# Performance work log

Measured on AMD Instinct MI355X. Metric: run time of the kernel, lower is better.

Reference implementation:

```python
import jax, jax.numpy as jnp
import numpy as np

N, H, S, D = 2, 8, 2048, 64

def setup_inputs() -> dict:
    key = jax.random.key(0)
    k1, k2, k3, k4 = jax.random.split(key, 4)
    queries = jax.random.normal(k1, (N, H, S, D), dtype=jnp.float32)
    keys = jax.random.normal(k2, (N, H, S, D), dtype=jnp.float32)
    values = jax.random.normal(k3, (N, H, S, D), dtype=jnp.float32)
    attn_mask = jax.random.randint(k4, (1, 1, S, S), 0, 2, dtype=jnp.int32)
    return {"queries": queries, "keys": keys, "values": values, "attn_mask": attn_mask}

def reference(queries, keys, values, attn_mask):
    # Faithful to the torch code: softmax over axis=2 (query/seq axis) for Q,
    # softmax over axis=1 (heads axis) for K, exactly as written.
    Q = jax.nn.softmax(queries, axis=2)
    K = jax.nn.softmax(keys, axis=1)
    attention_weights = jnp.einsum('nhqd,nhkd->nhqk', Q, K)  # [N,H,S,S]
    attention_weights = jnp.where(attn_mask == 0, -jnp.inf, attention_weights)
    attention_weights = jax.nn.softmax(attention_weights, axis=-1)
    context = jnp.einsum('nhqk,nhkd->nhqd', attention_weights, values)
    return context, attention_weights
```

## Files before the change

### kernel.cpp

```cpp
#include <hip/hip_runtime.h>

#define S 2048
#define Dh 64
#define NH 16
#define SD (S*Dh)
#define SSZ ((size_t)S*(size_t)S)

typedef __attribute__((ext_vector_type(4))) float f32x4;
typedef __attribute__((ext_vector_type(16))) float f32x16;
typedef __attribute__((ext_vector_type(8))) short s16x8;
typedef __attribute__((ext_vector_type(4))) unsigned int u32x4;

#define WSB_QSUM 0
#define WSB_RINV 4096
#define WSB_MASK 135168
#define WSB_QS   659456
#define WSB_KS   (WSB_QS + 4194304)
#define WSB_VT   (WSB_KS + 4194304)

__device__ __forceinline__ ushort f2bf(float x) {
    unsigned u = __builtin_bit_cast(unsigned, x);
    u = (u + 0x7fffu + ((u >> 16) & 1u)) >> 16;
    return (ushort)u;
}

__device__ __forceinline__ void gload_lds16(const ushort* g, ushort* l) {
    __builtin_amdgcn_global_load_lds(
        (const __attribute__((address_space(1))) unsigned int*)(const void*)g,
        (__attribute__((address_space(3))) unsigned int*)(void*)l,
        16, 0, 0);
}

__global__ void k_qsum(const float* __restrict__ q, float* __restrict__ qsum) {
    const int head  = blockIdx.x >> 5;
    const int chunk = blockIdx.x & 31;
    const int t = threadIdx.x;
    const int d = t & 63, sg = t >> 6;
    const float* qh = q + (size_t)head * SD;
    const int s0 = chunk * 64;
    float acc = 0.f;
#pragma unroll
    for (int i = 0; i < 16; ++i) {
        int s = s0 + sg + 4 * i;
        acc += __expf(qh[s * Dh + d]);
    }
    __shared__ float part[4][64];
    part[sg][d] = acc;
    __syncthreads();
    if (sg == 0)
        atomicAdd(&qsum[head * 64 + d], part[0][d] + part[1][d] + part[2][d] + part[3][d]);
}

__global__ void k_qnorm(const float* __restrict__ q, const float* __restrict__ qsum,
                        ushort* __restrict__ Qs) {
    const int gid = blockIdx.x * 256 + threadIdx.x;
    const int i0 = gid * 8;
    const int head = i0 >> 17;
    const int d0 = i0 & 63;
    const float4 a = ((const float4*)(q + i0))[0];
    const float4 b = ((const float4*)(q + i0))[1];
    const float* qs = qsum + head * 64 + d0;
    s16x8 o;
    o[0] = (short)f2bf(__expf(a.x) / qs[0]);
    o[1] = (short)f2bf(__expf(a.y) / qs[1]);
    o[2] = (short)f2bf(__expf(a.z) / qs[2]);
    o[3] = (short)f2bf(__expf(a.w) / qs[3]);
    o[4] = (short)f2bf(__expf(b.x) / qs[4]);
    o[5] = (short)f2bf(__expf(b.y) / qs[5]);
    o[6] = (short)f2bf(__expf(b.z) / qs[6]);
    o[7] = (short)f2bf(__expf(b.w) / qs[7]);
    *(s16x8*)(Qs + i0) = o;
}

__global__ void k_ksoft(const float* __restrict__ kin, ushort* __restrict__ Ks) {
    const int gid = blockIdx.x * 256 + threadIdx.x;
    const int n = gid >> 17;
    const int rem = gid & (SD - 1);
    const float* base = kin + (size_t)n * 8 * SD + rem;
    float x[8];
    float sum = 0.f;
#pragma unroll
    for (int h = 0; h < 8; ++h) { x[h] = __expf(base[(size_t)h * SD]); sum += x[h]; }
    const float inv = 1.f / sum;
    ushort* ob = Ks + (size_t)n * 8 * SD + rem;
#pragma unroll
    for (int h = 0; h < 8; ++h) ob[(size_t)h * SD] = f2bf(x[h] * inv);
}

__global__ void k_vt(const float* __restrict__ V, ushort* __restrict__ Vt) {
    const int head = blockIdx.x >> 5, kt = blockIdx.x & 31;
    const int t = threadIdx.x;
    __shared__ float sv[64 * 68];
    const float4* src = (const float4*)(V + (size_t)head * SD + (size_t)kt * 64 * 64);
#pragma unroll
    for (int i = 0; i < 4; ++i) {
        int idx = t + 256 * i;
        int row = idx >> 4, c4 = idx & 15;
        *(float4*)&sv[row * 68 + c4 * 4] = src[idx];
    }
    __syncthreads();
    const int d = t >> 2, seg = t & 3;
    s16x8 v0, v1;
#pragma unroll
    for (int j = 0; j < 8; ++j) v0[j] = (short)f2bf(sv[(seg * 16 + j) * 68 + d]);
#pragma unroll
    for (int j = 0; j < 8; ++j) v1[j] = (short)f2bf(sv[(seg * 16 + 8 + j) * 68 + d]);
    ushort* dst = Vt + (size_t)head * SD + (size_t)d * S + kt * 64 + seg * 16;
    *(s16x8*)dst = v0;
    *(s16x8*)(dst + 8) = v1;
}

__global__ void k_mask(const int* __restrict__ mask, unsigned long long* __restrict__ bmt) {
    const int t = threadIdx.x;
    const int g = blockIdx.x * 4 + (t >> 6);
    const int lane = t & 63;
#pragma unroll
    for (int it = 0; it < 16; ++it) {
        int w = g * 16 + it;
        int m = mask[(size_t)w * 64 + lane];
        unsigned long long b = __ballot(m != 0);
        if (lane == 0) bmt[(size_t)(w & 31) * S + (w >> 5)] = b;
    }
}

__global__ __launch_bounds__(256, 4) void k_ctx(
        const ushort* __restrict__ Qs, const ushort* __restrict__ Ks,
        const ushort* __restrict__ Vt, const unsigned long long* __restrict__ bmt,
        float* __restrict__ ctx, float* __restrict__ rinv) {
    const int head = blockIdx.x, qt = blockIdx.y;
    const int q0 = qt * 32;
    const int t = threadIdx.x;
    const int lane = t & 63, w = t >> 6;
    const int ql = lane & 31, hi = lane >> 5;
    const int q = q0 + ql;

    __shared__ __align__(16) char smem[37504];
    ushort* sK = (ushort*)smem;
    ushort* sV = (ushort*)(smem + 16384);
    float* redo  = (float*)smem;
    float* redrs = (float*)(smem + 36864);
    float* sInv  = (float*)(smem + 37376);

    const ushort* Qb = Qs + (size_t)head * SD;
    const ushort* Kb = Ks + (size_t)head * SD;
    const ushort* Vb = Vt + (size_t)head * SD;

    s16x8 bq[4];
#pragma unroll
    for (int s = 0; s < 4; ++s)
        bq[s] = *(const s16x8*)(Qb + (size_t)q * 64 + 16 * s + 8 * hi);

    f32x16 o0, o1;
#pragma unroll
    for (int r = 0; r < 16; ++r) { o0[r] = 0.f; o1[r] = 0.f; }
    float rs = 0.f;

    for (int mt = 0; mt < 16; ++mt) {
        const int k0 = mt * 128;
        __syncthreads();
#pragma unroll
        for (int i = 0; i < 4; ++i) {
            const int idx = t + 256 * i;
            const int row = idx >> 3, c = idx & 7;
            gload_lds16(Kb + (size_t)(k0 + row) * 64 + ((c ^ (row & 7)) * 8), &sK[idx * 8]);
        }
#pragma unroll
        for (int i = 0; i < 4; ++i) {
            const int idx = t + 256 * i;
            const int row = idx >> 4, c = idx & 15;
            gload_lds16(Vb + (size_t)row * S + k0 + ((c ^ (row & 7)) * 8), &sV[idx * 8]);
        }
        __syncthreads();

        f32x16 sc;
#pragma unroll
        for (int r = 0; r < 16; ++r) sc[r] = 0.f;
        const int arow = 32 * w + ql;
#pragma unroll
        for (int s = 0; s < 4; ++s) {
            const s16x8 ak = *(const s16x8*)&sK[arow * 64 + (((2 * s + hi) ^ (arow & 7)) * 8)];
            sc = __builtin_amdgcn_mfma_f32_32x32x16_bf16(ak, bq[s], sc, 0, 0, 0);
        }

        const unsigned long long m64 = bmt[(size_t)(2 * mt + (w >> 1)) * S + q];
        const unsigned mbits = (w & 1) ? (unsigned)(m64 >> 32) : (unsigned)m64;

        unsigned pk8[8];
        float rsum = 0.f;
#pragma unroll
        for (int g = 0; g < 8; ++g) {
            const int r0 = 2 * g;
            const int kb = (r0 & 3) + 8 * (r0 >> 2) + 4 * hi;
            const float e0 = ((mbits >> kb) & 1u) ? __expf(sc[r0]) : 0.f;
            const float e1 = ((mbits >> (kb + 1)) & 1u) ? __expf(sc[r0 + 1]) : 0.f;
            rsum += e0 + e1;
            pk8[g] = ((unsigned)f2bf(e1) << 16) | (unsigned)f2bf(e0);
        }
        rsum += __shfl_xor(rsum, 32);
        rs += rsum;

        const unsigned x1 = __shfl_xor(hi ? pk8[0] : pk8[2], 32);
        const unsigned x2 = __shfl_xor(hi ? pk8[1] : pk8[3], 32);
        const unsigned x3 = __shfl_xor(hi ? pk8[4] : pk8[6], 32);
        const unsigned x4 = __shfl_xor(hi ? pk8[5] : pk8[7], 32);
        const u32x4 w0 = hi ? (u32x4){x1, x2, pk8[2], pk8[3]}
                            : (u32x4){pk8[0], pk8[1], x1, x2};
        const u32x4 w1 = hi ? (u32x4){x3, x4, pk8[6], pk8[7]}
                            : (u32x4){pk8[4], pk8[5], x3, x4};
        const s16x8 pb0 = __builtin_bit_cast(s16x8, w0);
        const s16x8 pb1 = __builtin_bit_cast(s16x8, w1);

#pragma unroll
        for (int cs = 0; cs < 2; ++cs) {
            const s16x8 pbv = cs ? pb1 : pb0;
            {
                const int vrow = ql;
                const int ch = (4 * w + 2 * cs + hi) ^ (vrow & 7);
                const s16x8 av = *(const s16x8*)&sV[vrow * 128 + ch * 8];
                o0 = __builtin_amdgcn_mfma_f32_32x32x16_bf16(av, pbv, o0, 0, 0, 0);
            }
            {
                const int vrow = 32 + ql;
                const int ch = (4 * w + 2 * cs + hi) ^ (vrow & 7);
                const s16x8 av = *(const s16x8*)&sV[vrow * 128 + ch * 8];
                o1 = __builtin_amdgcn_mfma_f32_32x32x16_bf16(av, pbv, o1, 0, 0, 0);
            }
        }
    }

    __syncthreads();
    {
        float* dst = &redo[(w * 64 + lane) * 36];
#pragma unroll
        for (int g = 0; g < 4; ++g)
            *(f32x4*)&dst[4 * g] = (f32x4){o0[4*g], o0[4*g+1], o0[4*g+2], o0[4*g+3]};
#pragma unroll
        for (int g = 0; g < 4; ++g)
            *(f32x4*)&dst[16 + 4 * g] = (f32x4){o1[4*g], o1[4*g+1], o1[4*g+2], o1[4*g+3]};
        if (hi == 0) redrs[w * 32 + ql] = rs;
    }
    __syncthreads();
    if (t < 32) {
        const float inv = 1.f / (redrs[t] + redrs[32 + t] + redrs[64 + t] + redrs[96 + t]);
        rinv[head * S + q0 + t] = inv;
        sInv[t] = inv;
    }
    __syncthreads();
#pragma unroll
    for (int cc = 0; cc < 2; ++cc) {
        const int c = t + 256 * cc;
        const int l = c & 63, rq = c >> 6;
        f32x4 sum = *(const f32x4*)&redo[l * 36 + rq * 4];
#pragma unroll
        for (int ww = 1; ww < 4; ++ww)
            sum += *(const f32x4*)&redo[(ww * 64 + l) * 36 + rq * 4];
        const int qc = l & 31, hc = l >> 5;
        const int dtc = rq >> 2, rg = rq & 3;
        const int d0 = 32 * dtc + 4 * hc + 8 * rg;
        sum *= sInv[qc];
        *(f32x4*)(ctx + (size_t)head * SD + (size_t)(q0 + qc) * 64 + d0) = sum;
    }
}

__global__ __launch_bounds__(256, 4) void k_awrite(
        const ushort* __restrict__ Qs, const ushort* __restrict__ Ks,
        const unsigned long long* __restrict__ bmt, const float* __restrict__ rinv,
        float* __restrict__ A) {
    const int head = blockIdx.x, qt = blockIdx.y, kc = blockIdx.z;
    const int q0 = qt * 64;
    const int t = threadIdx.x;
    const int lane = t & 63, wv = t >> 6;
    const int lm = lane & 15, lg = lane >> 4;
    const int q = q0 + 16 * wv + lm;

    __shared__ __align__(16) char smem[33792];
    ushort* sK = (ushort*)smem;
    float* sP = (float*)(smem + 16384);

    const ushort* Qb = Qs + (size_t)head * SD;
    const ushort* Kb = Ks + (size_t)head * SD;
    float* Ah = A + (size_t)head * SSZ;

    auto stage = [&](int b, int k0) {
#pragma unroll
        for (int i = 0; i < 2; ++i) {
            const int idx = t + 256 * i;
            const int row = idx >> 3, seg = idx & 7;
            gload_lds16(Kb + (size_t)(k0 + row) * 64 + ((seg ^ (row & 7)) * 8),
                        &sK[b * 4096 + idx * 8]);
        }
    };

    s16x8 bq[2];
#pragma unroll
    for (int h = 0; h < 2; ++h)
        bq[h] = *(const s16x8*)(Qb + (size_t)q * 64 + 32 * h + 8 * lg);
    const float invr = rinv[head * S + q];
    float* sPw = &sP[wv * 16 * 68];

    stage(0, kc * 512);
    unsigned long long m64 = bmt[(size_t)(kc * 8) * S + q];
    __syncthreads();

    for (int kt8 = 0; kt8 < 8; ++kt8) {
        const int k0 = kc * 512 + kt8 * 64;
        const int cur = kt8 & 1;
        if (kt8 < 7) stage(cur ^ 1, k0 + 64);
        const unsigned long long m64n =
            (kt8 < 7) ? bmt[(size_t)((k0 >> 6) + 1) * S + q] : 0ULL;

        f32x4 sc[4];
#pragma unroll
        for (int j = 0; j < 4; ++j) sc[j] = (f32x4){0.f, 0.f, 0.f, 0.f};
#pragma unroll
        for (int h = 0; h < 2; ++h)
#pragma unroll
            for (int j = 0; j < 4; ++j) {
                s16x8 ak = *(const s16x8*)&sK[cur * 4096 + (16 * j + lm) * 64 +
                                              (((4 * h + lg) ^ (lm & 7)) * 8)];
                sc[j] = __builtin_amdgcn_mfma_f32_16x16x32_bf16(ak, bq[h], sc[j], 0, 0, 0);
            }

#pragma unroll
        for (int j = 0; j < 4; ++j) {
            f32x4 pv;
#pragma unroll
            for (int r = 0; r < 4; ++r) {
                const int b = 16 * j + 4 * lg + r;
                pv[r] = ((m64 >> b) & 1ULL) ? __expf(sc[j][r]) * invr : 0.f;
            }
            *(f32x4*)&sPw[lm * 68 + 16 * j + 4 * lg] = pv;
        }
#pragma unroll
        for (int pass = 0; pass < 4; ++pass) {
            const int rr = (lane >> 4) + 4 * pass;
            f32x4 pv = *(const f32x4*)&sPw[rr * 68 + (lane & 15) * 4];
            __builtin_nontemporal_store(pv,
                (f32x4*)&Ah[(size_t)(q0 + 16 * wv + rr) * S + k0 + (lane & 15) * 4]);
        }
        __syncthreads();
        m64 = m64n;
    }
}

extern "C" void kernel_launch(void* const* d_in, const int* in_sizes, int n_in,
                              void* d_out, int out_size, void* d_ws, size_t ws_size,
                              hipStream_t stream) {
    const float* q = (const float*)d_in[0];
    const float* k = (const float*)d_in[1];
    const float* v = (const float*)d_in[2];
    const int* mask = (const int*)d_in[3];
    float* out = (float*)d_out;
    char* ws = (char*)d_ws;

    float* qsum = (float*)(ws + WSB_QSUM);
    float* rinv = (float*)(ws + WSB_RINV);
    unsigned long long* bm = (unsigned long long*)(ws + WSB_MASK);
    ushort* Qs = (ushort*)(ws + WSB_QS);
    ushort* Ks = (ushort*)(ws + WSB_KS);
    ushort* Vt = (ushort*)(ws + WSB_VT);

    (void)hipMemsetAsync(d_ws, 0, 4096, stream);
    k_qsum<<<512, 256, 0, stream>>>(q, qsum);
    k_mask<<<1024, 256, 0, stream>>>(mask, bm);
    k_qnorm<<<1024, 256, 0, stream>>>(q, qsum, Qs);
    k_ksoft<<<1024, 256, 0, stream>>>(k, Ks);
    k_vt<<<512, 256, 0, stream>>>(v, Vt);
    k_ctx<<<dim3(16, 64), 256, 0, stream>>>(Qs, Ks, Vt, bm, out, rinv);
    k_awrite<<<dim3(16, 32, 4), 256, 0, stream>>>(Qs, Ks, bm, rinv, out + (size_t)NH * SD);
}
```

Before: 377.0 us.

## Store unnormalized bf16 probabilities in ctx kernel and rescale them for attention output

The ctx kernel now also writes its masked, exponentiated bf16 scores to a workspace buffer. The attention-weights kernel no longer recomputes QK^T with MFMA, the exp and the mask. It reads those packed values, multiplies them by the row inverse sum, transposes them through LDS and stores them in fp32. This trades a second pass of matrix math for an extra 128 MB of bf16 traffic (a write and a read), and it adds stores inside ctx's inner loop.

```diff
diff --git a/kernel.cpp b/kernel.cpp
--- a/kernel.cpp
+++ b/kernel.cpp
@@ -17,6 +17,7 @@
 #define WSB_QS   659456
 #define WSB_KS   (WSB_QS + 4194304)
 #define WSB_VT   (WSB_KS + 4194304)
+#define WSB_PR   13242368
 
 __device__ __forceinline__ ushort f2bf(float x) {
     unsigned u = __builtin_bit_cast(unsigned, x);
@@ -126,7 +127,7 @@
 __global__ __launch_bounds__(256, 4) void k_ctx(
         const ushort* __restrict__ Qs, const ushort* __restrict__ Ks,
         const ushort* __restrict__ Vt, const unsigned long long* __restrict__ bmt,
-        float* __restrict__ ctx, float* __restrict__ rinv) {
+        unsigned* __restrict__ Pr, float* __restrict__ ctx, float* __restrict__ rinv) {
     const int head = blockIdx.x, qt = blockIdx.y;
     const int q0 = qt * 32;
     const int t = threadIdx.x;
@@ -195,6 +196,12 @@
             const float e1 = ((mbits >> (kb + 1)) & 1u) ? __expf(sc[r0 + 1]) : 0.f;
             rsum += e0 + e1;
             pk8[g] = ((unsigned)f2bf(e1) << 16) | (unsigned)f2bf(e0);
+        }
+        {
+            unsigned* dst = Pr + ((size_t)head << 21) + ((size_t)qt << 15)
+                               + (mt << 11) + (w << 9) + lane * 4;
+            *(u32x4*)dst = (u32x4){pk8[0], pk8[1], pk8[2], pk8[3]};
+            *(u32x4*)(dst + 256) = (u32x4){pk8[4], pk8[5], pk8[6], pk8[7]};
         }
         rsum += __shfl_xor(rsum, 32);
         rs += rsum;
@@ -262,84 +269,46 @@
     }
 }
 
-__global__ __launch_bounds__(256, 4) void k_awrite(
-        const ushort* __restrict__ Qs, const ushort* __restrict__ Ks,
-        const unsigned long long* __restrict__ bmt, const float* __restrict__ rinv,
+__global__ __launch_bounds__(256, 8) void k_ascale(
+        const unsigned* __restrict__ Pr, const float* __restrict__ rinv,
         float* __restrict__ A) {
-    const int head = blockIdx.x, qt = blockIdx.y, kc = blockIdx.z;
-    const int q0 = qt * 64;
+    const int head = blockIdx.x, qg = blockIdx.y, kc = blockIdx.z;
+    const int q0 = qg * 32;
     const int t = threadIdx.x;
     const int lane = t & 63, wv = t >> 6;
-    const int lm = lane & 15, lg = lane >> 4;
-    const int q = q0 + 16 * wv + lm;
-
-    __shared__ __align__(16) char smem[33792];
-    ushort* sK = (ushort*)smem;
-    float* sP = (float*)(smem + 16384);
-
-    const ushort* Qb = Qs + (size_t)head * SD;
-    const ushort* Kb = Ks + (size_t)head * SD;
+    const int ql = lane & 31, lh = lane >> 5;
+
+    __shared__ __align__(16) float sPf[32][132];
+
+    const float invr = rinv[head * S + q0 + ql];
     float* Ah = A + (size_t)head * SSZ;
-
-    auto stage = [&](int b, int k0) {
-#pragma unroll
-        for (int i = 0; i < 2; ++i) {
-            const int idx = t + 256 * i;
-            const int row = idx >> 3, seg = idx & 7;
-            gload_lds16(Kb + (size_t)(k0 + row) * 64 + ((seg ^ (row & 7)) * 8),
-                        &sK[b * 4096 + idx * 8]);
-        }
-    };
-
-    s16x8 bq[2];
-#pragma unroll
-    for (int h = 0; h < 2; ++h)
-        bq[h] = *(const s16x8*)(Qb + (size_t)q * 64 + 32 * h + 8 * lg);
-    const float invr = rinv[head * S + q];
-    float* sPw = &sP[wv * 16 * 68];
-
-    stage(0, kc * 512);
-    unsigned long long m64 = bmt[(size_t)(kc * 8) * S + q];
-    __syncthreads();
-
-    for (int kt8 = 0; kt8 < 8; ++kt8) {
-        const int k0 = kc * 512 + kt8 * 64;
-        const int cur = kt8 & 1;
-        if (kt8 < 7) stage(cur ^ 1, k0 + 64);
-        const unsigned long long m64n =
-            (kt8 < 7) ? bmt[(size_t)((k0 >> 6) + 1) * S + q] : 0ULL;
-
-        f32x4 sc[4];
-#pragma unroll
-        for (int j = 0; j < 4; ++j) sc[j] = (f32x4){0.f, 0.f, 0.f, 0.f};
-#pragma unroll
-        for (int h = 0; h < 2; ++h)
-#pragma unroll
-            for (int j = 0; j < 4; ++j) {
-                s16x8 ak = *(const s16x8*)&sK[cur * 4096 + (16 * j + lm) * 64 +
-                                              (((4 * h + lg) ^ (lm & 7)) * 8)];
-                sc[j] = __builtin_amdgcn_mfma_f32_16x16x32_bf16(ak, bq[h], sc[j], 0, 0, 0);
-            }
-
+    const unsigned* baseh = Pr + ((size_t)head << 21) + ((size_t)qg << 15);
+
+    for (int m = 0; m < 8; ++m) {
+        const int mt = kc * 8 + m;
+        const unsigned* bb = baseh + (mt << 11) + (wv << 9);
+        const u32x4 a = *(const u32x4*)(bb + (32 * lh + ql) * 4);
+        const u32x4 b = *(const u32x4*)(bb + 256 + (32 * lh + ql) * 4);
 #pragma unroll
         for (int j = 0; j < 4; ++j) {
-            f32x4 pv;
-#pragma unroll
-            for (int r = 0; r < 4; ++r) {
-                const int b = 16 * j + 4 * lg + r;
-                pv[r] = ((m64 >> b) & 1ULL) ? __expf(sc[j][r]) * invr : 0.f;
-            }
-            *(f32x4*)&sPw[lm * 68 + 16 * j + 4 * lg] = pv;
-        }
-#pragma unroll
-        for (int pass = 0; pass < 4; ++pass) {
-            const int rr = (lane >> 4) + 4 * pass;
-            f32x4 pv = *(const f32x4*)&sPw[rr * 68 + (lane & 15) * 4];
-            __builtin_nontemporal_store(pv,
-                (f32x4*)&Ah[(size_t)(q0 + 16 * wv + rr) * S + k0 + (lane & 15) * 4]);
+            const unsigned ga = (j == 0) ? a[0] : (j == 1) ? a[2] : (j == 2) ? b[0] : b[2];
+            const unsigned gb = (j == 0) ? a[1] : (j == 1) ? a[3] : (j == 2) ? b[1] : b[3];
+            f32x4 v;
+            v[0] = __builtin_bit_cast(float, ga << 16) * invr;
+            v[1] = __builtin_bit_cast(float, ga & 0xFFFF0000u) * invr;
+            v[2] = __builtin_bit_cast(float, gb << 16) * invr;
+            v[3] = __builtin_bit_cast(float, gb & 0xFFFF0000u) * invr;
+            *(f32x4*)&sPf[ql][wv * 32 + 8 * j + 4 * lh] = v;
         }
         __syncthreads();
-        m64 = m64n;
+#pragma unroll
+        for (int rr = 0; rr < 4; ++rr) {
+            const int row = rr * 8 + (t >> 5);
+            const f32x4 vv = *(const f32x4*)&sPf[row][(t & 31) * 4];
+            __builtin_nontemporal_store(vv,
+                (f32x4*)&Ah[(size_t)(q0 + row) * S + mt * 128 + (t & 31) * 4]);
+        }
+        __syncthreads();
     }
 }
 
@@ -359,6 +328,7 @@
     ushort* Qs = (ushort*)(ws + WSB_QS);
     ushort* Ks = (ushort*)(ws + WSB_KS);
     ushort* Vt = (ushort*)(ws + WSB_VT);
+    unsigned* Pr = (unsigned*)(ws + WSB_PR);
 
     (void)hipMemsetAsync(d_ws, 0, 4096, stream);
     k_qsum<<<512, 256, 0, stream>>>(q, qsum);
@@ -366,6 +336,6 @@
     k_qnorm<<<1024, 256, 0, stream>>>(q, qsum, Qs);
     k_ksoft<<<1024, 256, 0, stream>>>(k, Ks);
     k_vt<<<512, 256, 0, stream>>>(v, Vt);
-    k_ctx<<<dim3(16, 64), 256, 0, stream>>>(Qs, Ks, Vt, bm, out, rinv);
-    k_awrite<<<dim3(16, 32, 4), 256, 0, stream>>>(Qs, Ks, bm, rinv, out + (size_t)NH * SD);
-}
+    k_ctx<<<dim3(16, 64), 256, 0, stream>>>(Qs, Ks, Vt, bm, Pr, out, rinv);
+    k_ascale<<<dim3(16, 64, 2), 256, 0, stream>>>(Pr, rinv, out + (size_t)NH * SD);
+}
```

Result: slower. 387.4 us (+2.8%).

## Single-buffer K tile and stage probabilities as bf16 to raise awrite occupancy

Applied to the files above, without the earlier changes.

The attention-weight write kernel drops K double buffering and stores the probability tile in shared memory as packed bf16 instead of fp32. This shrinks LDS per block from about 33KB to 17KB, and launch bounds are raised from 4 to 6 blocks per CU. Each thread now writes 64 contiguous bytes per row when it expands the bf16 values back to fp32 for the nontemporal stores. In exchange, K loads for the next tile are no longer overlapped with compute, and the written attention weights are rounded to bf16 precision, which may exceed tolerance.

```diff
diff --git a/kernel.cpp b/kernel.cpp
--- a/kernel.cpp
+++ b/kernel.cpp
@@ -262,7 +262,7 @@
     }
 }
 
-__global__ __launch_bounds__(256, 4) void k_awrite(
+__global__ __launch_bounds__(256, 6) void k_awrite(
         const ushort* __restrict__ Qs, const ushort* __restrict__ Ks,
         const unsigned long long* __restrict__ bmt, const float* __restrict__ rinv,
         float* __restrict__ A) {
@@ -273,21 +273,21 @@
     const int lm = lane & 15, lg = lane >> 4;
     const int q = q0 + 16 * wv + lm;
 
-    __shared__ __align__(16) char smem[33792];
+    __shared__ __align__(16) char smem[17408];
     ushort* sK = (ushort*)smem;
-    float* sP = (float*)(smem + 16384);
+    unsigned* sP = (unsigned*)(smem + 8192);
 
     const ushort* Qb = Qs + (size_t)head * SD;
     const ushort* Kb = Ks + (size_t)head * SD;
     float* Ah = A + (size_t)head * SSZ;
 
-    auto stage = [&](int b, int k0) {
+    auto stage = [&](int k0) {
 #pragma unroll
         for (int i = 0; i < 2; ++i) {
             const int idx = t + 256 * i;
             const int row = idx >> 3, seg = idx & 7;
             gload_lds16(Kb + (size_t)(k0 + row) * 64 + ((seg ^ (row & 7)) * 8),
-                        &sK[b * 4096 + idx * 8]);
+                        &sK[idx * 8]);
         }
     };
 
@@ -296,18 +296,13 @@
     for (int h = 0; h < 2; ++h)
         bq[h] = *(const s16x8*)(Qb + (size_t)q * 64 + 32 * h + 8 * lg);
     const float invr = rinv[head * S + q];
-    float* sPw = &sP[wv * 16 * 68];
-
-    stage(0, kc * 512);
+
+    stage(kc * 512);
     unsigned long long m64 = bmt[(size_t)(kc * 8) * S + q];
-    __syncthreads();
 
     for (int kt8 = 0; kt8 < 8; ++kt8) {
         const int k0 = kc * 512 + kt8 * 64;
-        const int cur = kt8 & 1;
-        if (kt8 < 7) stage(cur ^ 1, k0 + 64);
-        const unsigned long long m64n =
-            (kt8 < 7) ? bmt[(size_t)((k0 >> 6) + 1) * S + q] : 0ULL;
+        __syncthreads();
 
         f32x4 sc[4];
 #pragma unroll
@@ -316,29 +311,52 @@
         for (int h = 0; h < 2; ++h)
 #pragma unroll
             for (int j = 0; j < 4; ++j) {
-                s16x8 ak = *(const s16x8*)&sK[cur * 4096 + (16 * j + lm) * 64 +
+                s16x8 ak = *(const s16x8*)&sK[(16 * j + lm) * 64 +
                                               (((4 * h + lg) ^ (lm & 7)) * 8)];
                 sc[j] = __builtin_amdgcn_mfma_f32_16x16x32_bf16(ak, bq[h], sc[j], 0, 0, 0);
             }
 
+        unsigned* prow = &sP[(16 * wv + lm) * 36];
 #pragma unroll
         for (int j = 0; j < 4; ++j) {
-            f32x4 pv;
-#pragma unroll
-            for (int r = 0; r < 4; ++r) {
-                const int b = 16 * j + 4 * lg + r;
-                pv[r] = ((m64 >> b) & 1ULL) ? __expf(sc[j][r]) * invr : 0.f;
-            }
-            *(f32x4*)&sPw[lm * 68 + 16 * j + 4 * lg] = pv;
-        }
-#pragma unroll
-        for (int pass = 0; pass < 4; ++pass) {
-            const int rr = (lane >> 4) + 4 * pass;
-            f32x4 pv = *(const f32x4*)&sPw[rr * 68 + (lane & 15) * 4];
-            __builtin_nontemporal_store(pv,
-                (f32x4*)&Ah[(size_t)(q0 + 16 * wv + rr) * S + k0 + (lane & 15) * 4]);
-        }
+            const int b0 = 16 * j + 4 * lg;
+            const float p0 = ((m64 >> b0) & 1ULL) ? __expf(sc[j][0]) * invr : 0.f;
+            const float p1 = ((m64 >> (b0 + 1)) & 1ULL) ? __expf(sc[j][1]) * invr : 0.f;
+            const float p2 = ((m64 >> (b0 + 2)) & 1ULL) ? __expf(sc[j][2]) * invr : 0.f;
+            const float p3 = ((m64 >> (b0 + 3)) & 1ULL) ? __expf(sc[j][3]) * invr : 0.f;
+            prow[8 * j + 2 * lg]     = ((unsigned)f2bf(p1) << 16) | (unsigned)f2bf(p0);
+            prow[8 * j + 2 * lg + 1] = ((unsigned)f2bf(p3) << 16) | (unsigned)f2bf(p2);
+        }
+        const unsigned long long m64n =
+            (kt8 < 7) ? bmt[(size_t)((k0 >> 6) + 1) * S + q] : 0ULL;
+
         __syncthreads();
+        if (kt8 < 7) stage(k0 + 64);
+
+        const int row = t >> 2, seg = t & 3;
+        const u32x4 pa = *(const u32x4*)&sP[row * 36 + seg * 8];
+        const u32x4 pb = *(const u32x4*)&sP[row * 36 + seg * 8 + 4];
+        float* dst = &Ah[(size_t)(q0 + row) * S + k0 + seg * 16];
+#pragma unroll
+        for (int g = 0; g < 2; ++g) {
+            const unsigned ua = g ? pa[2] : pa[0], ub = g ? pa[3] : pa[1];
+            f32x4 v;
+            v[0] = __builtin_bit_cast(float, ua << 16);
+            v[1] = __builtin_bit_cast(float, ua & 0xFFFF0000u);
+            v[2] = __builtin_bit_cast(float, ub << 16);
+            v[3] = __builtin_bit_cast(float, ub & 0xFFFF0000u);
+            __builtin_nontemporal_store(v, (f32x4*)(dst + 4 * g));
+        }
+#pragma unroll
+        for (int g = 0; g < 2; ++g) {
+            const unsigned ua = g ? pb[2] : pb[0], ub = g ? pb[3] : pb[1];
+            f32x4 v;
+            v[0] = __builtin_bit_cast(float, ua << 16);
+            v[1] = __builtin_bit_cast(float, ua & 0xFFFF0000u);
+            v[2] = __builtin_bit_cast(float, ub << 16);
+            v[3] = __builtin_bit_cast(float, ub & 0xFFFF0000u);
+            __builtin_nontemporal_store(v, (f32x4*)(dst + 8 + 4 * g));
+        }
         m64 = m64n;
     }
 }
```

After: 782.5 us. +107.6%, slower.
